# Kernel optimization log

Measured on AMD Instinct MI355X. Metric: run time of the kernel, lower is better.

Reference implementation:

```python
import jax, jax.numpy as jnp
import numpy as np

B, S, D_IN = 2, 2048, 2048
NUM_HEADS, NUM_KV_GROUPS, HEAD_DIM = 32, 8, 64
GROUP_SIZE = NUM_HEADS // NUM_KV_GROUPS  # 4
D_OUT = NUM_HEADS * HEAD_DIM  # 2048


def setup_inputs() -> dict:
    key = jax.random.key(0)
    k1, k2, k3, k4, k5 = jax.random.split(key, 5)
    scale_in = 1.0 / np.sqrt(D_IN)
    scale_out = 1.0 / np.sqrt(D_OUT)
    return {
        "x": jax.random.normal(k1, (B, S, D_IN), dtype=jnp.float32),
        # Linear weights stored torch-style as (out_features, in_features); y = x @ W.T
        "Wq": jax.random.uniform(k2, (D_OUT, D_IN), minval=-scale_in, maxval=scale_in, dtype=jnp.float32),
        "Wk": jax.random.uniform(k3, (NUM_KV_GROUPS * HEAD_DIM, D_IN), minval=-scale_in, maxval=scale_in, dtype=jnp.float32),
        "Wv": jax.random.uniform(k4, (NUM_KV_GROUPS * HEAD_DIM, D_IN), minval=-scale_in, maxval=scale_in, dtype=jnp.float32),
        "Wo": jax.random.uniform(k5, (D_IN, D_OUT), minval=-scale_out, maxval=scale_out, dtype=jnp.float32),
    }


def reference(x, Wq, Wk, Wv, Wo):
    b, s, _ = x.shape
    # Projections
    q = (x @ Wq.T).reshape(b, s, NUM_KV_GROUPS, GROUP_SIZE, HEAD_DIM)  # [b,s,g,r,d]
    k = (x @ Wk.T).reshape(b, s, NUM_KV_GROUPS, HEAD_DIM)              # [b,s,g,d]
    v = (x @ Wv.T).reshape(b, s, NUM_KV_GROUPS, HEAD_DIM)
    # Scores: broadcast each KV group over its group of query heads
    # (equivalent to repeat_interleave of K/V along head dim)
    scores = jnp.einsum("bqgrd,bkgd->bgrqk", q, k) / np.sqrt(HEAD_DIM).astype(jnp.float32)
    causal = jnp.tril(jnp.ones((s, s), dtype=bool))  # True = keep
    scores = jnp.where(causal, scores, jnp.finfo(scores.dtype).min)
    attn = jax.nn.softmax(scores, axis=-1)  # [b,g,r,q,k]
    ctx = jnp.einsum("bgrqk,bkgd->bqgrd", attn, v).reshape(b, s, D_OUT)
    out = ctx @ Wo.T
    # new_kv_cache (un-expanded keys/values, layout [b, g, s, d])
    keys = k.transpose(0, 2, 1, 3)
    values = v.transpose(0, 2, 1, 3)
    return out, (keys, values)
```

## Files before the change

kernel.cpp:

```cpp
#include <hip/hip_runtime.h>


#define B_   2
#define S_   2048
#define DIN  2048
#define NH   32
#define NKV  8
#define HD   64
#define DOUT 2048
#define NQKV 3072

#define QSCALE 0.18033688f

typedef short bf16x8 __attribute__((ext_vector_type(8)));
typedef short bf16x4 __attribute__((ext_vector_type(4)));
typedef float f32x4  __attribute__((ext_vector_type(4)));

__device__ __forceinline__ unsigned short f2bf(float f) {
  unsigned int u = __float_as_uint(f);
  u += 0x7fff + ((u >> 16) & 1);
  return (unsigned short)(u >> 16);
}

__device__ __forceinline__ f32x4 mfma16(bf16x4 a, bf16x4 b, f32x4 c) {
#if __has_builtin(__builtin_amdgcn_mfma_f32_16x16x16bf16_1k)
  return __builtin_amdgcn_mfma_f32_16x16x16bf16_1k(a, b, c, 0, 0, 0);
#else
  asm volatile("v_mfma_f32_16x16x16_bf16 %0, %1, %2, %0" : "+v"(c) : "v"(a), "v"(b));
  return c;
#endif
}

__device__ __forceinline__ void gld_lds16(const void* gptr, void* lptr) {
  __builtin_amdgcn_global_load_lds(
      (const __attribute__((address_space(1))) unsigned int*)gptr,
      (__attribute__((address_space(3))) unsigned int*)lptr,
      16, 0, 0);
}

__device__ __forceinline__ bf16x8 ds_read128(const unsigned short* p) {
  bf16x8 r;
  asm volatile("ds_read_b128 %0, %1"
               : "=v"(r)
               : "v"((const __attribute__((address_space(3))) unsigned short*)p));
  return r;
}

#define BAR() __builtin_amdgcn_s_barrier()
#define SB()  __builtin_amdgcn_sched_barrier(0)
#define VMCNT(n) asm volatile("s_waitcnt vmcnt(" #n ")")
#define LGKM0()                                   \
  do {                                            \
    asm volatile("s_waitcnt lgkmcnt(0)");         \
    __builtin_amdgcn_sched_barrier(0);            \
  } while (0)

__global__ __launch_bounds__(256) void cvt_all(
    const float* __restrict__ x,  const float* __restrict__ Wq,
    const float* __restrict__ Wk, const float* __restrict__ Wv,
    const float* __restrict__ Wo,
    unsigned short* __restrict__ xbf, unsigned short* __restrict__ wqkv,
    unsigned short* __restrict__ wobf) {
  int i = blockIdx.x * blockDim.x + threadIdx.x;
  const float* src; unsigned short* dst; int off;
  if (i < 2097152)      { src = x;  dst = xbf;                  off = i; }
  else if (i < 3145728) { src = Wq; dst = wqkv;                 off = i - 2097152; }
  else if (i < 3407872) { src = Wk; dst = wqkv + 2048 * 2048;   off = i - 3145728; }
  else if (i < 3670016) { src = Wv; dst = wqkv + 2560 * 2048;   off = i - 3407872; }
  else                  { src = Wo; dst = wobf;                 off = i - 3670016; }
  float4 f = ((const float4*)src)[off];
  ushort4 o;
  o.x = f2bf(f.x); o.y = f2bf(f.y); o.z = f2bf(f.z); o.w = f2bf(f.w);
  ((ushort4*)dst)[off] = o;
}

#define MMA_PHASE(MH, NHH, AF, BF)                                              \
  do {                                                                          \
    __builtin_amdgcn_s_setprio(1);                                              \
    _Pragma("unroll")                                                           \
    for (int kk = 0; kk < 2; ++kk)                                              \
      _Pragma("unroll")                                                         \
      for (int mr = 0; mr < 4; ++mr)                                            \
        _Pragma("unroll")                                                       \
        for (int nr = 0; nr < NR; ++nr)                                         \
          acc[(MH) * 4 + mr][(NHH) * NR + nr] =                                 \
              __builtin_amdgcn_mfma_f32_16x16x32_bf16(                          \
                  AF[mr][kk], BF[nr][kk], acc[(MH) * 4 + mr][(NHH) * NR + nr],  \
                  0, 0, 0);                                                     \
    __builtin_amdgcn_s_setprio(0);                                              \
  } while (0)

#define WAITW()                                   \
  do {                                            \
    if constexpr (BN == 256) VMCNT(4);            \
    else                     VMCNT(3);            \
  } while (0)

template <int MODE, int BN, int NTN>
__global__ __launch_bounds__(512, 2) void gemm8p(
    const unsigned short* __restrict__ A,
    const unsigned short* __restrict__ Bm,
    int K,
    unsigned short* __restrict__ qbf,
    unsigned short* __restrict__ kbf,
    unsigned short* __restrict__ vtbf,
    float* __restrict__ kout,
    float* __restrict__ vout,
    float* __restrict__ cout) {
  constexpr int NR = BN / 128;
  constexpr int BHROW = BN / 2;
  __shared__ unsigned short As[2][256 * 64];
  __shared__ unsigned short Bs[2][BN * 64];

  const int tid  = threadIdx.x;
  const int lane = tid & 63;
  const int wave = tid >> 6;
  const int wm   = wave >> 2;
  const int wn   = wave & 3;
  const int quad = lane >> 4;
  const int r16  = lane & 15;

  const int NT = K / 64;

  const int nwg = gridDim.x;
  const int id  = blockIdx.x;
  const int sid = (id & 7) * (nwg >> 3) + (id >> 3);
  const int by  = sid / NTN;
  const int bx  = sid % NTN;
  const int aRowBase = by * 256;
  const int bColBase = bx * BN;

  f32x4 zero = {0.f, 0.f, 0.f, 0.f};
  f32x4 acc[8][2 * NR];
#pragma unroll
  for (int i = 0; i < 8; ++i)
#pragma unroll
    for (int j = 0; j < 2 * NR; ++j) acc[i][j] = zero;

  auto stageA = [&](int dbuf, int h, int t) {
    const int tt = t < NT ? t : NT - 1;
    const int k0 = tt * 64;
#pragma unroll
    for (int i = 0; i < 2; ++i) {
      const int chunk = (i * 8 + wave) * 64 + lane;
      const int row = chunk >> 3;
      const int slot = chunk & 7;
      const int gc = (slot ^ (row & 7)) * 8;
      gld_lds16(A + (size_t)(aRowBase + h * 128 + row) * K + k0 + gc,
                &As[dbuf][h * 8192 + (i * 8 + wave) * 512]);
    }
  };
  auto stageB = [&](int dbuf, int h, int t) {
    const int tt = t < NT ? t : NT - 1;
    const int k0 = tt * 64;
    if constexpr (BN == 256) {
#pragma unroll
      for (int i = 0; i < 2; ++i) {
        const int chunk = (i * 8 + wave) * 64 + lane;
        const int row = chunk >> 3;
        const int slot = chunk & 7;
        const int gc = (slot ^ (row & 7)) * 8;
        gld_lds16(Bm + (size_t)(bColBase + h * 128 + row) * K + k0 + gc,
                  &Bs[dbuf][h * 8192 + (i * 8 + wave) * 512]);
      }
    } else {
      const int chunk = wave * 64 + lane;
      const int row = chunk >> 3;
      const int slot = chunk & 7;
      const int gc = (slot ^ (row & 7)) * 8;
      gld_lds16(Bm + (size_t)(bColBase + h * 64 + row) * K + k0 + gc,
                &Bs[dbuf][h * 4096 + wave * 512]);
    }
  };

  bf16x8 afA[4][2];
  bf16x8 afB[4][2];
  bf16x8 b0[NR][2];
  bf16x8 b1[NR][2];

  auto readA = [&](int sbuf, int mh, bf16x8 (&dst)[4][2]) {
#pragma unroll
    for (int mr = 0; mr < 4; ++mr)
#pragma unroll
      for (int kk = 0; kk < 2; ++kk) {
        const int row = mh * 128 + wm * 64 + mr * 16 + r16;
        const int slot = (kk * 4 + quad) ^ (r16 & 7);
        dst[mr][kk] = ds_read128(&As[sbuf][row * 64 + slot * 8]);
      }
  };
  auto readB = [&](int sbuf, int nh, bf16x8 (&dst)[NR][2]) {
#pragma unroll
    for (int nr = 0; nr < NR; ++nr)
#pragma unroll
      for (int kk = 0; kk < 2; ++kk) {
        const int row = nh * BHROW + wn * (BN / 8) + nr * 16 + r16;
        const int slot = (kk * 4 + quad) ^ (r16 & 7);
        dst[nr][kk] = ds_read128(&Bs[sbuf][row * 64 + slot * 8]);
      }
  };

  stageA(0, 0, 0);
  stageB(0, 0, 0);
  stageB(0, 1, 0);
  stageA(0, 1, 0);
  stageA(1, 0, 1);
  stageB(1, 0, 1);
  WAITW();
  BAR();
  stageB(1, 1, 1);
  readA(0, 0, afA);
  readB(0, 0, b0);
  SB();

  const int NIT = NT / 2;
  for (int i = 0; i < NIT; ++i) {
    const int e2 = 2 * i + 2, o2 = 2 * i + 3;

    stageA(1, 1, 2 * i + 1);
    BAR();
    LGKM0();
    readB(0, 1, b1); SB();
    MMA_PHASE(0, 0, afA, b0);
    BAR();

    stageA(0, 0, e2);
    BAR();
    LGKM0();
    readA(0, 1, afB); SB();
    MMA_PHASE(0, 1, afA, b1);
    BAR();

    stageB(0, 0, e2);
    BAR();
    LGKM0();
    MMA_PHASE(1, 0, afB, b0);
    WAITW();
    BAR();

    stageB(0, 1, e2);
    BAR();
    readA(1, 0, afA);
    readB(1, 0, b0); SB();
    MMA_PHASE(1, 1, afB, b1);
    BAR();

    stageA(0, 1, e2);
    BAR();
    LGKM0();
    readB(1, 1, b1); SB();
    MMA_PHASE(0, 0, afA, b0);
    BAR();

    stageA(1, 0, o2);
    BAR();
    LGKM0();
    readA(1, 1, afB); SB();
    MMA_PHASE(0, 1, afA, b1);
    BAR();

    stageB(1, 0, o2);
    BAR();
    LGKM0();
    MMA_PHASE(1, 0, afB, b0);
    WAITW();
    BAR();

    stageB(1, 1, o2);
    BAR();
    readA(0, 0, afA);
    readB(0, 0, b0); SB();
    MMA_PHASE(1, 1, afB, b1);
    BAR();
  }
  asm volatile("s_waitcnt vmcnt(0) lgkmcnt(0)");

#pragma unroll
  for (int mi = 0; mi < 8; ++mi) {
    const int mh = mi >> 2, mr = mi & 3;
#pragma unroll
    for (int ni = 0; ni < 2 * NR; ++ni) {
      const int nh = ni / NR, nr = ni % NR;
      const int rowb = aRowBase + mh * 128 + wm * 64 + mr * 16 + quad * 4;
      const int col  = bColBase +
                       (BN == 256 ? nh * 128 + wn * 32 + nr * 16
                                  : nh * 64 + wn * 16) + r16;
#pragma unroll
      for (int reg = 0; reg < 4; ++reg) {
        const float v = acc[mi][ni][reg];
        const int m = rowb + reg;
        if (MODE == 1) {
          cout[(size_t)m * DOUT + col] = v;
        } else {
          if (col < 2048) {
            qbf[(size_t)m * DOUT + col] = f2bf(v * QSCALE);
          } else if (col < 2560) {
            const int gg = (col - 2048) >> 6, d = col & 63;
            const int b = m >> 11, s = m & 2047;
            const size_t idx = ((size_t)(b * NKV + gg) * S_ + s) * HD + d;
            kbf[idx]  = f2bf(v);
            kout[idx] = v;
          } else {
            const int gg = (col - 2560) >> 6, d = col & 63;
            const int b = m >> 11, s = m & 2047;
            vtbf[((size_t)(b * NKV + gg) * HD + d) * S_ + s]  = f2bf(v);
            vout[((size_t)(b * NKV + gg) * S_ + s) * HD + d] = v;
          }
        }
      }
    }
  }
}

__global__ __launch_bounds__(512, 4) void attn_kernel(
    const unsigned short* __restrict__ Q,
    const unsigned short* __restrict__ Kb,
    const unsigned short* __restrict__ VT,
    unsigned short* __restrict__ ctx) {
  __shared__ unsigned short Kbuf[2][4096];
  __shared__ unsigned short Vbuf[2][4096];

  const int tid  = threadIdx.x;
  const int lane = tid & 63;
  const int wave = tid >> 6;
  const int grp  = wave >> 2;
  const int hw   = wave & 3;
  const int quad = lane >> 4;
  const int r16  = lane & 15;
  const int g    = blockIdx.y;
  const int b    = blockIdx.z;
  const int h    = g * 4 + hw;
  const int pairI = blockIdx.x;
  const int q0     = grp ? pairI * 32 : (63 - pairI) * 32;
  const int nT_own = grp ? pairI / 2 + 1 : (63 - pairI) / 2 + 1;
  const int nTa    = (63 - pairI) / 2 + 1;

  const unsigned short* Kh  = Kb + (size_t)(b * NKV + g) * S_ * HD;
  const unsigned short* VTh = VT + (size_t)(b * NKV + g) * HD * S_;

  const int srow   = lane >> 3;
  const int schunk = (lane & 7) ^ srow;

  bf16x8 aq[2][2];
#pragma unroll
  for (int mt = 0; mt < 2; ++mt)
#pragma unroll
    for (int kk = 0; kk < 2; ++kk)
      aq[mt][kk] = *(const bf16x8*)(Q + (size_t)(b * S_ + q0 + mt * 16 + r16) * DOUT +
                                    h * HD + kk * 32 + quad * 8);

  bf16x4 ones4;
#pragma unroll
  for (int i = 0; i < 4; ++i) ones4[i] = (short)0x3F80;

  f32x4 zero = {0.f, 0.f, 0.f, 0.f};
  f32x4 o[2][4];
  f32x4 l[2];
#pragma unroll
  for (int mt = 0; mt < 2; ++mt) {
    l[mt] = zero;
#pragma unroll
    for (int dt = 0; dt < 4; ++dt) o[mt][dt] = zero;
  }

  auto stage = [&](int buf, int kt) {
    const int kbase = kt * 64;
    gld_lds16(Kh + (size_t)(kbase + wave * 8 + srow) * HD + schunk * 8,
              &Kbuf[buf][wave * 512]);
    gld_lds16(VTh + (size_t)(wave * 8 + srow) * S_ + kbase + schunk * 8,
              &Vbuf[buf][wave * 512]);
  };

  stage(0, 0);
  __syncthreads();

  for (int kt = 0; kt < nTa; ++kt) {
    const int buf = kt & 1;
    if (kt + 1 < nTa) stage(buf ^ 1, kt + 1);

    if (kt < nT_own) {
      bf16x8 bk[4][2];
#pragma unroll
      for (int nt = 0; nt < 4; ++nt)
#pragma unroll
        for (int kk = 0; kk < 2; ++kk) {
          const int seg = nt * 2 + (r16 >> 3), r = r16 & 7;
          const int slot = (kk * 4 + quad) ^ r;
          bk[nt][kk] = *(const bf16x8*)&Kbuf[buf][seg * 512 + r * 64 + slot * 8];
        }

      const bool last = (kt == nT_own - 1);
#pragma unroll
      for (int mt = 0; mt < 2; ++mt) {
        f32x4 st[4];
#pragma unroll
        for (int nt = 0; nt < 4; ++nt) st[nt] = zero;
#pragma unroll
        for (int kk = 0; kk < 2; ++kk)
#pragma unroll
          for (int nt = 0; nt < 4; ++nt)
            st[nt] = __builtin_amdgcn_mfma_f32_16x16x32_bf16(bk[nt][kk], aq[mt][kk], st[nt], 0, 0, 0);

        bf16x4 pf[4];
#pragma unroll
        for (int nt = 0; nt < 4; ++nt) {
#pragma unroll
          for (int r = 0; r < 4; ++r) {
            float s = st[nt][r];
            if (last) {
              const int key = kt * 64 + nt * 16 + quad * 4 + r;
              const int row = q0 + mt * 16 + r16;
              if (key > row) s = -1e38f;
            }
            const float p = __builtin_amdgcn_exp2f(s);
            pf[nt][r] = (short)(__float_as_uint(p) >> 16);
          }
        }
#pragma unroll
        for (int nt = 0; nt < 4; ++nt) l[mt] = mfma16(pf[nt], ones4, l[mt]);
#pragma unroll
        for (int dt = 0; dt < 4; ++dt) {
          const int seg = dt * 2 + (r16 >> 3), r = r16 & 7;
#pragma unroll
          for (int nt = 0; nt < 4; ++nt) {
            const int slot = (nt * 2 + (quad >> 1)) ^ r;
            bf16x4 bv = *(const bf16x4*)&Vbuf[buf][seg * 512 + r * 64 + slot * 8 + (quad & 1) * 4];
            o[mt][dt] = mfma16(pf[nt], bv, o[mt][dt]);
          }
        }
      }
    }

    __syncthreads();
  }

#pragma unroll
  for (int mt = 0; mt < 2; ++mt) {
    f32x4 rl;
#pragma unroll
    for (int r = 0; r < 4; ++r) rl[r] = __builtin_amdgcn_rcpf(l[mt][r]);
#pragma unroll
    for (int dt = 0; dt < 4; ++dt)
#pragma unroll
      for (int r = 0; r < 4; ++r) {
        const int qq = q0 + mt * 16 + quad * 4 + r;
        ctx[(size_t)(b * S_ + qq) * DOUT + h * HD + dt * 16 + r16] =
            f2bf(o[mt][dt][r] * rl[r]);
      }
  }
}

extern "C" void kernel_launch(void* const* d_in, const int* in_sizes, int n_in,
                              void* d_out, int out_size, void* d_ws, size_t ws_size,
                              hipStream_t stream) {
  const float* x  = (const float*)d_in[0];
  const float* Wq = (const float*)d_in[1];
  const float* Wk = (const float*)d_in[2];
  const float* Wv = (const float*)d_in[3];
  const float* Wo = (const float*)d_in[4];

  float* out  = (float*)d_out;
  float* keys = out + (size_t)B_ * S_ * DOUT;
  float* vals = keys + (size_t)B_ * NKV * S_ * HD;

  unsigned short* xbf  = (unsigned short*)d_ws;
  unsigned short* wqkv = xbf  + (size_t)B_ * S_ * DIN;
  unsigned short* wobf = wqkv + (size_t)NQKV * DIN;
  unsigned short* qbf  = wobf + (size_t)DIN * DOUT;
  unsigned short* kbf  = qbf  + (size_t)B_ * S_ * DOUT;
  unsigned short* vtbf = kbf  + (size_t)B_ * NKV * S_ * HD;
  unsigned short* ctx  = vtbf + (size_t)B_ * NKV * S_ * HD;

  cvt_all<<<dim3(4718592 / 256), dim3(256), 0, stream>>>(x, Wq, Wk, Wv, Wo,
                                                         xbf, wqkv, wobf);

  gemm8p<0, 256, 12><<<dim3(192), dim3(512), 0, stream>>>(
      xbf, wqkv, DIN, qbf, kbf, vtbf, keys, vals, nullptr);

  attn_kernel<<<dim3(32, NKV, B_), dim3(512), 0, stream>>>(qbf, kbf, vtbf, ctx);

  gemm8p<1, 128, 16><<<dim3(256), dim3(512), 0, stream>>>(
      ctx, wobf, DOUT, nullptr, nullptr, nullptr, nullptr, nullptr, out);
}
```

Baseline: 290.6 us.

## Triple-buffer attention K/V staging and software-pipeline LDS reads with MFMAs

Moves the attention kernel's K/V LDS staging from double to triple buffering, prefetching two tiles ahead with vmcnt-based waits in place of a full __syncthreads. Inside the tile loop it also reads the V fragments ahead one d-tile at a time, using explicit lgkmcnt waits so ds_reads overlap with MFMAs. The goal is to hide global-load and LDS latency. In exchange it uses more LDS per block, which may lower occupancy, and it adds redundant loads of the last tile at the tail of the loop.

```diff
diff --git a/kernel.cpp b/kernel.cpp
--- a/kernel.cpp
+++ b/kernel.cpp
@@ -45,15 +45,23 @@
                : "v"((const __attribute__((address_space(3))) unsigned short*)p));
   return r;
 }
+__device__ __forceinline__ bf16x4 ds_read64(const unsigned short* p) {
+  bf16x4 r;
+  asm volatile("ds_read_b64 %0, %1"
+               : "=v"(r)
+               : "v"((const __attribute__((address_space(3))) unsigned short*)p));
+  return r;
+}
 
 #define BAR() __builtin_amdgcn_s_barrier()
 #define SB()  __builtin_amdgcn_sched_barrier(0)
 #define VMCNT(n) asm volatile("s_waitcnt vmcnt(" #n ")")
-#define LGKM0()                                   \
+#define LGKM(n)                                   \
   do {                                            \
-    asm volatile("s_waitcnt lgkmcnt(0)");         \
+    asm volatile("s_waitcnt lgkmcnt(" #n ")");    \
     __builtin_amdgcn_sched_barrier(0);            \
   } while (0)
+#define LGKM0() LGKM(0)
 
 __global__ __launch_bounds__(256) void cvt_all(
     const float* __restrict__ x,  const float* __restrict__ Wq,
@@ -316,8 +324,8 @@
     const unsigned short* __restrict__ Kb,
     const unsigned short* __restrict__ VT,
     unsigned short* __restrict__ ctx) {
-  __shared__ unsigned short Kbuf[2][4096];
-  __shared__ unsigned short Vbuf[2][4096];
+  __shared__ unsigned short Kbuf[3][4096];
+  __shared__ unsigned short Vbuf[3][4096];
 
   const int tid  = threadIdx.x;
   const int lane = tid & 63;
@@ -347,6 +355,7 @@
     for (int kk = 0; kk < 2; ++kk)
       aq[mt][kk] = *(const bf16x8*)(Q + (size_t)(b * S_ + q0 + mt * 16 + r16) * DOUT +
                                     h * HD + kk * 32 + quad * 8);
+  asm volatile("" :: "v"(aq[0][0]), "v"(aq[0][1]), "v"(aq[1][0]), "v"(aq[1][1]));
 
   bf16x4 ones4;
 #pragma unroll
@@ -371,13 +380,17 @@
   };
 
   stage(0, 0);
-  __syncthreads();
-
+  stage(1, 1);
+  VMCNT(2);
+  BAR();
+
+  int bufC = 0, bufN = 1, bufP = 2;
   for (int kt = 0; kt < nTa; ++kt) {
-    const int buf = kt & 1;
-    if (kt + 1 < nTa) stage(buf ^ 1, kt + 1);
+    const int tpre = (kt + 2 < nTa) ? kt + 2 : nTa - 1;
+    stage(bufP, tpre);
 
     if (kt < nT_own) {
+      const bool last = (kt == nT_own - 1);
       bf16x8 bk[4][2];
 #pragma unroll
       for (int nt = 0; nt < 4; ++nt)
@@ -385,12 +398,24 @@
         for (int kk = 0; kk < 2; ++kk) {
           const int seg = nt * 2 + (r16 >> 3), r = r16 & 7;
           const int slot = (kk * 4 + quad) ^ r;
-          bk[nt][kk] = *(const bf16x8*)&Kbuf[buf][seg * 512 + r * 64 + slot * 8];
+          bk[nt][kk] = ds_read128(&Kbuf[bufC][seg * 512 + r * 64 + slot * 8]);
         }
 
-      const bool last = (kt == nT_own - 1);
+      bf16x4 bvA[4], bvB[4];
+      auto readV = [&](bf16x4 (&dst)[4], int dt) {
+#pragma unroll
+        for (int nt = 0; nt < 4; ++nt) {
+          const int seg = dt * 2 + (r16 >> 3), r = r16 & 7;
+          const int slot = (nt * 2 + (quad >> 1)) ^ r;
+          dst[nt] = ds_read64(&Vbuf[bufC][seg * 512 + r * 64 + slot * 8 +
+                                          (quad & 1) * 4]);
+        }
+      };
+
 #pragma unroll
       for (int mt = 0; mt < 2; ++mt) {
+        readV(bvA, 0);
+        if (mt == 0) LGKM(4);
         f32x4 st[4];
 #pragma unroll
         for (int nt = 0; nt < 4; ++nt) st[nt] = zero;
@@ -417,21 +442,27 @@
         }
 #pragma unroll
         for (int nt = 0; nt < 4; ++nt) l[mt] = mfma16(pf[nt], ones4, l[mt]);
-#pragma unroll
-        for (int dt = 0; dt < 4; ++dt) {
-          const int seg = dt * 2 + (r16 >> 3), r = r16 & 7;
-#pragma unroll
-          for (int nt = 0; nt < 4; ++nt) {
-            const int slot = (nt * 2 + (quad >> 1)) ^ r;
-            bf16x4 bv = *(const bf16x4*)&Vbuf[buf][seg * 512 + r * 64 + slot * 8 + (quad & 1) * 4];
-            o[mt][dt] = mfma16(pf[nt], bv, o[mt][dt]);
-          }
-        }
+
+        readV(bvB, 1); LGKM(4);
+#pragma unroll
+        for (int nt = 0; nt < 4; ++nt) o[mt][0] = mfma16(pf[nt], bvA[nt], o[mt][0]);
+        readV(bvA, 2); LGKM(4);
+#pragma unroll
+        for (int nt = 0; nt < 4; ++nt) o[mt][1] = mfma16(pf[nt], bvB[nt], o[mt][1]);
+        readV(bvB, 3); LGKM(4);
+#pragma unroll
+        for (int nt = 0; nt < 4; ++nt) o[mt][2] = mfma16(pf[nt], bvA[nt], o[mt][2]);
+        LGKM(0);
+#pragma unroll
+        for (int nt = 0; nt < 4; ++nt) o[mt][3] = mfma16(pf[nt], bvB[nt], o[mt][3]);
       }
     }
 
-    __syncthreads();
+    VMCNT(2);
+    BAR();
+    const int t = bufC; bufC = bufN; bufN = bufP; bufP = t;
   }
+  VMCNT(0);
 
 #pragma unroll
   for (int mt = 0; mt < 2; ++mt) {
```

Result: slower. 432.3 us (+48.8%).

## Split attention KV tiles across wave pairs and merge partial sums via LDS

Applied to the files above, without the earlier changes.

Each attention block now handles one 32-row query tile instead of pairing a short and a long tile. Two waves per head split the key tiles between them, even and odd, with double-buffered staging of two tiles per round. Their partial outputs and row sums are combined through shared memory at the end. This doubles the grid and shortens the serial per-wave KV loop, at the cost of more LDS (64KB), lower occupancy bounds and an extra reduction step. The wave-level work imbalance from the old causal pairing is replaced by block-level imbalance across the grid.

```diff
diff --git a/kernel.cpp b/kernel.cpp
--- a/kernel.cpp
+++ b/kernel.cpp
@@ -49,11 +49,12 @@
 #define BAR() __builtin_amdgcn_s_barrier()
 #define SB()  __builtin_amdgcn_sched_barrier(0)
 #define VMCNT(n) asm volatile("s_waitcnt vmcnt(" #n ")")
-#define LGKM0()                                   \
+#define LGKM(n)                                   \
   do {                                            \
-    asm volatile("s_waitcnt lgkmcnt(0)");         \
+    asm volatile("s_waitcnt lgkmcnt(" #n ")");    \
     __builtin_amdgcn_sched_barrier(0);            \
   } while (0)
+#define LGKM0() LGKM(0)
 
 __global__ __launch_bounds__(256) void cvt_all(
     const float* __restrict__ x,  const float* __restrict__ Wq,
@@ -311,28 +312,27 @@
   }
 }
 
-__global__ __launch_bounds__(512, 4) void attn_kernel(
+__global__ __launch_bounds__(512, 2) void attn_kernel(
     const unsigned short* __restrict__ Q,
     const unsigned short* __restrict__ Kb,
     const unsigned short* __restrict__ VT,
     unsigned short* __restrict__ ctx) {
-  __shared__ unsigned short Kbuf[2][4096];
-  __shared__ unsigned short Vbuf[2][4096];
+  __shared__ unsigned short smem[32768];
 
   const int tid  = threadIdx.x;
   const int lane = tid & 63;
   const int wave = tid >> 6;
-  const int grp  = wave >> 2;
-  const int hw   = wave & 3;
+  const int hw   = wave >> 1;
+  const int p    = wave & 1;
   const int quad = lane >> 4;
   const int r16  = lane & 15;
+  const int j    = 63 - blockIdx.x;
   const int g    = blockIdx.y;
   const int b    = blockIdx.z;
   const int h    = g * 4 + hw;
-  const int pairI = blockIdx.x;
-  const int q0     = grp ? pairI * 32 : (63 - pairI) * 32;
-  const int nT_own = grp ? pairI / 2 + 1 : (63 - pairI) / 2 + 1;
-  const int nTa    = (63 - pairI) / 2 + 1;
+  const int q0   = j * 32;
+  const int ntiles  = j / 2 + 1;
+  const int nrounds = (ntiles + 1) / 2;
 
   const unsigned short* Kh  = Kb + (size_t)(b * NKV + g) * S_ * HD;
   const unsigned short* VTh = VT + (size_t)(b * NKV + g) * HD * S_;
@@ -362,22 +362,32 @@
     for (int dt = 0; dt < 4; ++dt) o[mt][dt] = zero;
   }
 
-  auto stage = [&](int buf, int kt) {
-    const int kbase = kt * 64;
-    gld_lds16(Kh + (size_t)(kbase + wave * 8 + srow) * HD + schunk * 8,
-              &Kbuf[buf][wave * 512]);
-    gld_lds16(VTh + (size_t)(wave * 8 + srow) * S_ + kbase + schunk * 8,
-              &Vbuf[buf][wave * 512]);
+  auto stage_pair = [&](int d, int s) {
+    const int t0 = 2 * s;
+    const int t1 = (2 * s + 1 < ntiles) ? 2 * s + 1 : ntiles - 1;
+    unsigned short* k0 = smem + (d * 2 + 0) * 4096;
+    unsigned short* k1 = smem + (d * 2 + 1) * 4096;
+    unsigned short* v0 = smem + 16384 + (d * 2 + 0) * 4096;
+    unsigned short* v1 = smem + 16384 + (d * 2 + 1) * 4096;
+    gld_lds16(Kh + (size_t)(t0 * 64 + wave * 8 + srow) * HD + schunk * 8, k0 + wave * 512);
+    gld_lds16(Kh + (size_t)(t1 * 64 + wave * 8 + srow) * HD + schunk * 8, k1 + wave * 512);
+    gld_lds16(VTh + (size_t)(wave * 8 + srow) * S_ + t0 * 64 + schunk * 8, v0 + wave * 512);
+    gld_lds16(VTh + (size_t)(wave * 8 + srow) * S_ + t1 * 64 + schunk * 8, v1 + wave * 512);
   };
 
-  stage(0, 0);
+  stage_pair(0, 0);
   __syncthreads();
 
-  for (int kt = 0; kt < nTa; ++kt) {
-    const int buf = kt & 1;
-    if (kt + 1 < nTa) stage(buf ^ 1, kt + 1);
-
-    if (kt < nT_own) {
+  for (int s = 0; s < nrounds; ++s) {
+    const int d = s & 1;
+    if (s + 1 < nrounds) stage_pair(d ^ 1, s + 1);
+
+    const int t = 2 * s + p;
+    if (t < ntiles) {
+      const unsigned short* Kc = smem + (d * 2 + p) * 4096;
+      const unsigned short* Vc = smem + 16384 + (d * 2 + p) * 4096;
+      const bool last = (t == ntiles - 1);
+
       bf16x8 bk[4][2];
 #pragma unroll
       for (int nt = 0; nt < 4; ++nt)
@@ -385,10 +395,9 @@
         for (int kk = 0; kk < 2; ++kk) {
           const int seg = nt * 2 + (r16 >> 3), r = r16 & 7;
           const int slot = (kk * 4 + quad) ^ r;
-          bk[nt][kk] = *(const bf16x8*)&Kbuf[buf][seg * 512 + r * 64 + slot * 8];
+          bk[nt][kk] = *(const bf16x8*)&Kc[seg * 512 + r * 64 + slot * 8];
         }
 
-      const bool last = (kt == nT_own - 1);
 #pragma unroll
       for (int mt = 0; mt < 2; ++mt) {
         f32x4 st[4];
@@ -405,14 +414,14 @@
         for (int nt = 0; nt < 4; ++nt) {
 #pragma unroll
           for (int r = 0; r < 4; ++r) {
-            float s = st[nt][r];
+            float s2 = st[nt][r];
             if (last) {
-              const int key = kt * 64 + nt * 16 + quad * 4 + r;
+              const int key = t * 64 + nt * 16 + quad * 4 + r;
               const int row = q0 + mt * 16 + r16;
-              if (key > row) s = -1e38f;
+              if (key > row) s2 = -1e38f;
             }
-            const float p = __builtin_amdgcn_exp2f(s);
-            pf[nt][r] = (short)(__float_as_uint(p) >> 16);
+            const float pp = __builtin_amdgcn_exp2f(s2);
+            pf[nt][r] = (short)(__float_as_uint(pp) >> 16);
           }
         }
 #pragma unroll
@@ -423,7 +432,7 @@
 #pragma unroll
           for (int nt = 0; nt < 4; ++nt) {
             const int slot = (nt * 2 + (quad >> 1)) ^ r;
-            bf16x4 bv = *(const bf16x4*)&Vbuf[buf][seg * 512 + r * 64 + slot * 8 + (quad & 1) * 4];
+            bf16x4 bv = *(const bf16x4*)&Vc[seg * 512 + r * 64 + slot * 8 + (quad & 1) * 4];
             o[mt][dt] = mfma16(pf[nt], bv, o[mt][dt]);
           }
         }
@@ -433,19 +442,49 @@
     __syncthreads();
   }
 
-#pragma unroll
-  for (int mt = 0; mt < 2; ++mt) {
-    f32x4 rl;
-#pragma unroll
-    for (int r = 0; r < 4; ++r) rl[r] = __builtin_amdgcn_rcpf(l[mt][r]);
-#pragma unroll
-    for (int dt = 0; dt < 4; ++dt)
-#pragma unroll
-      for (int r = 0; r < 4; ++r) {
-        const int qq = q0 + mt * 16 + quad * 4 + r;
-        ctx[(size_t)(b * S_ + qq) * DOUT + h * HD + dt * 16 + r16] =
-            f2bf(o[mt][dt][r] * rl[r]);
-      }
+  float* sm = (float*)smem;
+  float* basep = sm + ((size_t)(hw * 64 + lane)) * 41;
+  if (p == 1) {
+#pragma unroll
+    for (int mt = 0; mt < 2; ++mt)
+#pragma unroll
+      for (int dt = 0; dt < 4; ++dt)
+#pragma unroll
+        for (int r = 0; r < 4; ++r)
+          basep[(mt * 4 + dt) * 4 + r] = o[mt][dt][r];
+#pragma unroll
+    for (int mt = 0; mt < 2; ++mt)
+#pragma unroll
+      for (int r = 0; r < 4; ++r)
+        basep[32 + mt * 4 + r] = l[mt][r];
+  }
+  __syncthreads();
+  if (p == 0) {
+#pragma unroll
+    for (int mt = 0; mt < 2; ++mt) {
+#pragma unroll
+      for (int dt = 0; dt < 4; ++dt)
+#pragma unroll
+        for (int r = 0; r < 4; ++r)
+          o[mt][dt][r] += basep[(mt * 4 + dt) * 4 + r];
+#pragma unroll
+      for (int r = 0; r < 4; ++r)
+        l[mt][r] += basep[32 + mt * 4 + r];
+    }
+#pragma unroll
+    for (int mt = 0; mt < 2; ++mt) {
+      f32x4 rl;
+#pragma unroll
+      for (int r = 0; r < 4; ++r) rl[r] = __builtin_amdgcn_rcpf(l[mt][r]);
+#pragma unroll
+      for (int dt = 0; dt < 4; ++dt)
+#pragma unroll
+        for (int r = 0; r < 4; ++r) {
+          const int qq = q0 + mt * 16 + quad * 4 + r;
+          ctx[(size_t)(b * S_ + qq) * DOUT + h * HD + dt * 16 + r16] =
+              f2bf(o[mt][dt][r] * rl[r]);
+        }
+    }
   }
 }
 
@@ -476,7 +515,7 @@
   gemm8p<0, 256, 12><<<dim3(192), dim3(512), 0, stream>>>(
       xbf, wqkv, DIN, qbf, kbf, vtbf, keys, vals, nullptr);
 
-  attn_kernel<<<dim3(32, NKV, B_), dim3(512), 0, stream>>>(qbf, kbf, vtbf, ctx);
+  attn_kernel<<<dim3(64, NKV, B_), dim3(512), 0, stream>>>(qbf, kbf, vtbf, ctx);
 
   gemm8p<1, 128, 16><<<dim3(256), dim3(512), 0, stream>>>(
       ctx, wobf, DOUT, nullptr, nullptr, nullptr, nullptr, nullptr, out);
```

Result: slower. 326.8 us (+12.5%).
